# Kernel optimization log

Measured on AMD Instinct MI355X. Metric: run time of the kernel, lower is better.

Reference implementation:

```python
import jax, jax.numpy as jnp
import numpy as np
from functools import partial

B, T, P, W = 32, 4096, 512, 128
NMEL, FILT, PDIM, K = 80, 256, 64, 9
PAD = (K - 1) // 2  # original uses (kernel[0][0]-1)//2 for both convs
EPS = 1e-5


def setup_inputs() -> dict:
    key = jax.random.key(0)
    ks = jax.random.split(key, 8)
    inp = {}
    inp["mask"] = jnp.zeros((B, P), dtype=bool)
    inp["mels"] = jax.random.normal(ks[0], (B, T, NMEL), dtype=jnp.float32)
    inp["mel_mask"] = jnp.zeros((B, T), dtype=bool)
    # uniform segments: 8 frames per phone (sum == T), 4 phones per word (sum == P)
    inp["durations"] = jnp.full((B, P), T // P, dtype=jnp.int32)
    inp["word_phone_len"] = jnp.full((B, W), P // W, dtype=jnp.int32)
    s1 = 1.0 / np.sqrt(NMEL * K)
    s2 = 1.0 / np.sqrt(FILT * K)
    s3 = 1.0 / np.sqrt(FILT)
    inp["conv1_w"] = jax.random.normal(ks[1], (FILT, NMEL, K), dtype=jnp.float32) * s1
    inp["conv1_b"] = jnp.zeros((FILT,), dtype=jnp.float32)
    inp["ln1_g"] = jnp.ones((FILT,), dtype=jnp.float32)
    inp["ln1_b"] = jnp.zeros((FILT,), dtype=jnp.float32)
    inp["conv2_w"] = jax.random.normal(ks[2], (FILT, FILT, K), dtype=jnp.float32) * s2
    inp["conv2_b"] = jnp.zeros((FILT,), dtype=jnp.float32)
    inp["ln2_g"] = jnp.ones((FILT,), dtype=jnp.float32)
    inp["ln2_b"] = jnp.zeros((FILT,), dtype=jnp.float32)
    inp["w1"] = jax.random.normal(ks[3], (FILT, FILT), dtype=jnp.float32) * s3
    inp["b1"] = jnp.zeros((FILT,), dtype=jnp.float32)
    inp["w2"] = jax.random.normal(ks[4], (FILT, PDIM), dtype=jnp.float32) * s3
    inp["b2"] = jnp.zeros((PDIM,), dtype=jnp.float32)
    return inp


def conv1d(x, w, b):
    # x: [B, T, Cin], w: [Cout, Cin, K] -> [B, T, Cout]
    y = jax.lax.conv_general_dilated(x.transpose(0, 2, 1), w, (1,), [(PAD, PAD)])
    return y.transpose(0, 2, 1) + b


def layernorm(x, g, b):
    m = jnp.mean(x, axis=-1, keepdims=True)
    v = jnp.mean(jnp.square(x - m), axis=-1, keepdims=True)
    return (x - m) * jax.lax.rsqrt(v + EPS) * g + b


def seg_mean(feat, lens, n_seg):
    # feat: [L, D], lens: [S] -> [n_seg, D] segment means
    bounds = jnp.cumsum(lens)
    ids = jnp.searchsorted(bounds, jnp.arange(feat.shape[0]), side="right")
    s = jax.ops.segment_sum(feat, ids, num_segments=n_seg)
    cnt = jnp.maximum(lens, 1).astype(feat.dtype)
    return s / cnt[:, None]


def expand_words(word_emb, wlens, n_out):
    # word_emb: [W, D]; scatter each word embedding across its phones -> [n_out, D]
    bounds = jnp.cumsum(wlens)
    wid = jnp.searchsorted(bounds, jnp.arange(n_out), side="right")
    return word_emb[jnp.clip(wid, 0, word_emb.shape[0] - 1)]


def reference(mask, mels, mel_mask, durations, word_phone_len,
              conv1_w, conv1_b, ln1_g, ln1_b, conv2_w, conv2_b, ln2_g, ln2_b,
              w1, b1, w2, b2):
    x = conv1d(mels, conv1_w, conv1_b)
    x = layernorm(jax.nn.relu(x), ln1_g, ln1_b)
    x = conv1d(x, conv2_w, conv2_b)
    x = layernorm(jax.nn.relu(x), ln2_g, ln2_b)  # [B, T, FILT]
    # token-wise (phone) mean pool over mel frames
    x = jax.vmap(partial(seg_mean, n_seg=P))(x, durations)  # [B, P, FILT]
    # word-level mean pool over phones
    x = jax.vmap(partial(seg_mean, n_seg=W))(x, word_phone_len)  # [B, W, FILT]
    x = jax.nn.relu(x @ w1 + b1)
    x = jax.nn.relu(x @ w2 + b2)  # [B, W, PDIM]
    # expand word embeddings back to phone level
    x = jax.vmap(partial(expand_words, n_out=P))(x, word_phone_len)  # [B, P, PDIM]
    x = jnp.where(mask[..., None], 0.0, x)
    return x
```

## Files before the change

### kernel.cpp

```cpp
#include <hip/hip_runtime.h>
#include <hip/hip_fp16.h>
#include <stdint.h>

#define B_ 32
#define T_ 4096
#define P_ 512
#define W_ 128
#define NMEL 80
#define FILT 256
#define PDIM 64
#define KW 9
#define TP8 (T_ + 8)
#define MSTR 104
#define YSTR 264
#define EPS 1e-5f

typedef unsigned short u16;
typedef __attribute__((ext_vector_type(8))) short short8;
typedef __attribute__((ext_vector_type(4))) float f32x4;

typedef const __attribute__((address_space(1))) uint32_t* gptr_t;
typedef __attribute__((address_space(3))) uint32_t* lptr_t;

__device__ __forceinline__ u16 f2h(float v){ return __half_as_ushort(__float2half(v)); }

#define MFMA16(accv, av, bv) \
  asm volatile("v_mfma_f32_16x16x32_f16 %0, %1, %2, %0" : "+v"(accv) : "v"(av), "v"(bv))

__global__ void pack_w(const float* __restrict__ w1, const float* __restrict__ w2,
                       u16* __restrict__ Wp1, u16* __restrict__ Wp2){
  int i = blockIdx.x * 256 + threadIdx.x;
  const int N1 = KW * 12 * FILT;
  const int N2 = KW * 32 * FILT;
  if (i < N1){
    int tap = i / (12*FILT); int r = i - tap*12*FILT; int kg = r / FILT; int co = r - kg*FILT;
    short8 v;
    #pragma unroll
    for (int e=0;e<8;e++){
      int ci = kg*8 + e;
      float x = (ci < NMEL) ? w1[(co*NMEL + ci)*KW + tap] : 0.f;
      v[e] = (short)f2h(x);
    }
    *(short8*)(Wp1 + (size_t)i*8) = v;
  } else if (i < N1 + N2){
    int j = i - N1;
    int tap = j / (32*FILT); int r = j - tap*32*FILT; int kg = r / FILT; int co = r - kg*FILT;
    short8 v;
    #pragma unroll
    for (int e=0;e<8;e++){
      int ci = kg*8 + e;
      v[e] = (short)f2h(w2[(co*FILT + ci)*KW + tap]);
    }
    *(short8*)(Wp2 + (size_t)j*8) = v;
  }
}

__global__ void prep_mels(const float* __restrict__ mels, u16* __restrict__ melsPad){
  int idx = blockIdx.x * 256 + threadIdx.x;
  if (idx >= B_*TP8*MSTR) return;
  int c = idx % MSTR; int r = idx / MSTR; int row = r % TP8; int b = r / TP8;
  float v = 0.f;
  int t = row - 4;
  if (t >= 0 && t < T_ && c < NMEL) v = mels[((size_t)b*T_ + t)*NMEL + c];
  melsPad[idx] = f2h(v);
}

__global__ void prep_seg(const int* __restrict__ dur, const int* __restrict__ wpl,
                         int* __restrict__ dcum, int* __restrict__ wcum,
                         int* __restrict__ pid, int* __restrict__ wid,
                         u16* __restrict__ y1Pad){
  int b = blockIdx.x; int tid = threadIdx.x;
  __shared__ int dc[P_];
  __shared__ int wc[W_];
  if (tid == 0){ int run=0; for (int p=0;p<P_;p++){ run += dur[b*P_+p]; dc[p]=run; dcum[b*P_+p]=run; } }
  if (tid == 1){ int run=0; for (int w=0;w<W_;w++){ run += wpl[b*W_+w]; wc[w]=run; wcum[b*W_+w]=run; } }
  __syncthreads();
  for (int t=tid; t<T_; t+=256){
    int lo=0, hi=P_;
    while (lo < hi){ int mid=(lo+hi)>>1; if (dc[mid] > t) hi=mid; else lo=mid+1; }
    pid[b*T_+t] = lo;
  }
  for (int p=tid; p<P_; p+=256){
    int lo=0, hi=W_;
    while (lo < hi){ int mid=(lo+hi)>>1; if (wc[mid] > p) hi=mid; else lo=mid+1; }
    wid[b*P_+p] = min(lo, W_-1);
  }
  for (int i=tid; i<8*YSTR; i+=256){
    int rr = i / YSTR; int cc = i - rr*YSTR;
    int row = (rr < 4) ? rr : (T_ + rr);
    y1Pad[((size_t)b*TP8 + row)*YSTR + cc] = 0;
  }
}

__global__ __launch_bounds__(256, 2) void conv1_k(
    const u16* __restrict__ melsPad, const u16* __restrict__ Wp1,
    const float* __restrict__ bias, const float* __restrict__ lng,
    const float* __restrict__ lnb, u16* __restrict__ y1Pad){
  __shared__ __align__(16) u16 sA[14336];
  __shared__ __align__(16) u16 sB[2][8192];
  const int tid = threadIdx.x;
  const int wave = tid >> 6, lane = tid & 63, lo = lane & 15, hi = lane >> 4;
  const int b = blockIdx.y, t0 = blockIdx.x * 128;

  {
    const char* gA = (const char*)(melsPad + ((size_t)b*TP8 + t0)*MSTR);
    #pragma unroll
    for (int it=0; it<7; ++it)
      __builtin_amdgcn_global_load_lds((gptr_t)(gA + it*4096 + tid*16),
                                       (lptr_t)((char*)sA + it*4096 + (wave<<10)), 16, 0, 0);
  }
  {
    const char* gW = (const char*)Wp1;
    #pragma unroll
    for (int it=0; it<4; ++it)
      __builtin_amdgcn_global_load_lds((gptr_t)(gW + it*4096 + tid*16),
                                       (lptr_t)((char*)sB[0] + it*4096 + (wave<<10)), 16, 0, 0);
  }

  f32x4 acc[8][4];
  #pragma unroll
  for (int m=0;m<8;m++)
    #pragma unroll
    for (int n=0;n<4;n++) acc[m][n] = (f32x4){0.f,0.f,0.f,0.f};

  __syncthreads();
  for (int cc=0; cc<27; ++cc){
    if (cc < 26){
      int nx = cc + 1;
      const char* gW = (const char*)(Wp1 + (size_t)((nx/3)*12 + (nx%3)*4)*FILT*8);
      char* ldsB = (char*)sB[nx & 1];
      #pragma unroll
      for (int it=0; it<4; ++it)
        __builtin_amdgcn_global_load_lds((gptr_t)(gW + it*4096 + tid*16),
                                         (lptr_t)(ldsB + it*4096 + (wave<<10)), 16, 0, 0);
    }
    const int tap = cc / 3, s = cc % 3;
    const u16* bufB = sB[cc & 1];
    short8 av[8], wv[4];
    #pragma unroll
    for (int m=0;m<8;m++)
      av[m] = *(const short8*)(sA + (m*16 + lo + tap)*MSTR + s*32 + hi*8);
    #pragma unroll
    for (int n=0;n<4;n++)
      wv[n] = *(const short8*)(bufB + ((size_t)hi*FILT + wave*64 + n*16 + lo)*8);
    #pragma unroll
    for (int m=0;m<8;m++)
      #pragma unroll
      for (int n=0;n<4;n++)
        MFMA16(acc[m][n], av[m], wv[n]);
    __syncthreads();
  }
  asm volatile("s_nop 7\n\ts_nop 7" :: );

  float* sred  = (float*)sB;
  float* sred2 = sred + 512;
  float* smean = sred2 + 512;
  float* srstd = smean + 128;

  float bcol[4], gcol[4], btcol[4];
  #pragma unroll
  for (int n=0;n<4;n++){
    int c = wave*64 + n*16 + lo;
    bcol[n]=bias[c]; gcol[n]=lng[c]; btcol[n]=lnb[c];
  }
  #pragma unroll
  for (int m=0;m<8;m++){
    #pragma unroll
    for (int jj=0;jj<4;jj++){
      float s=0.f, q=0.f;
      #pragma unroll
      for (int n=0;n<4;n++){
        float v = fmaxf(acc[m][n][jj] + bcol[n], 0.f);
        s += v; q += v*v;
      }
      #pragma unroll
      for (int off=1; off<16; off<<=1){ s += __shfl_xor(s, off); q += __shfl_xor(q, off); }
      if (lo == 0){ int r = m*16 + hi*4 + jj; sred[r*4+wave] = s; sred2[r*4+wave] = q; }
    }
  }
  __syncthreads();
  if (tid < 128){
    float ss=0.f, qq=0.f;
    #pragma unroll
    for (int w2=0; w2<4; w2++){ ss += sred[tid*4+w2]; qq += sred2[tid*4+w2]; }
    float mean = ss * (1.f/FILT);
    float var  = qq * (1.f/FILT) - mean*mean;
    smean[tid] = mean;
    srstd[tid] = rsqrtf(fmaxf(var, 0.f) + EPS);
  }
  __syncthreads();
  #pragma unroll
  for (int m=0;m<8;m++){
    float mn[4], rs[4];
    #pragma unroll
    for (int jj=0;jj<4;jj++){ int r = m*16+hi*4+jj; mn[jj]=smean[r]; rs[jj]=srstd[r]; }
    #pragma unroll
    for (int jj=0;jj<4;jj++){
      int r = m*16 + hi*4 + jj;
      #pragma unroll
      for (int n=0;n<4;n++){
        float v = fmaxf(acc[m][n][jj] + bcol[n], 0.f);
        float o = (v - mn[jj])*rs[jj]*gcol[n] + btcol[n];
        y1Pad[((size_t)b*TP8 + 4 + t0 + r)*YSTR + wave*64 + n*16 + lo] = f2h(o);
      }
    }
  }
}

__global__ __launch_bounds__(512, 2) void conv2_k(
    const u16* __restrict__ y1Pad, const u16* __restrict__ Wp2,
    const float* __restrict__ bias, const float* __restrict__ lng,
    const float* __restrict__ lnb, const int* __restrict__ pid,
    float* __restrict__ ps){
  __shared__ __align__(16) u16 sA[36864];
  __shared__ __align__(16) u16 sB[2][16384];
  __shared__ int pidT[128];
  const int tid = threadIdx.x;
  const int wave = tid >> 6, lane = tid & 63, lo = lane & 15, hi = lane >> 4;
  const int wr = wave >> 2, wc = wave & 3;
  const int b = blockIdx.y, t0 = blockIdx.x * 128;

  if (tid < 128) pidT[tid] = pid[b*T_ + t0 + tid];
  {
    const char* gA = (const char*)(y1Pad + ((size_t)b*TP8 + t0)*YSTR);
    #pragma unroll
    for (int it=0; it<9; ++it)
      __builtin_amdgcn_global_load_lds((gptr_t)(gA + it*8192 + tid*16),
                                       (lptr_t)((char*)sA + it*8192 + (wave<<10)), 16, 0, 0);
  }
  {
    const char* gW = (const char*)Wp2;
    #pragma unroll
    for (int it=0; it<4; ++it)
      __builtin_amdgcn_global_load_lds((gptr_t)(gW + it*8192 + tid*16),
                                       (lptr_t)((char*)sB[0] + it*8192 + (wave<<10)), 16, 0, 0);
  }

  f32x4 acc[4][4];
  #pragma unroll
  for (int m=0;m<4;m++)
    #pragma unroll
    for (int n=0;n<4;n++) acc[m][n] = (f32x4){0.f,0.f,0.f,0.f};

  __syncthreads();
  for (int cc=0; cc<36; ++cc){
    if (cc < 35){
      int nx = cc + 1;
      const char* gW = (const char*)(Wp2 + (size_t)((nx>>2)*32 + (nx&3)*8)*FILT*8);
      char* ldsB = (char*)sB[nx & 1];
      #pragma unroll
      for (int it=0; it<4; ++it)
        __builtin_amdgcn_global_load_lds((gptr_t)(gW + it*8192 + tid*16),
                                         (lptr_t)(ldsB + it*8192 + (wave<<10)), 16, 0, 0);
    }
    const int tap = cc >> 2, sblk = cc & 3;
    const u16* bufB = sB[cc & 1];
    #pragma unroll
    for (int s2=0; s2<2; ++s2){
      const int sg = sblk*2 + s2;
      short8 av[4], wv[4];
      #pragma unroll
      for (int m=0;m<4;m++)
        av[m] = *(const short8*)(sA + (wr*64 + m*16 + lo + tap)*YSTR + sg*32 + hi*8);
      #pragma unroll
      for (int n=0;n<4;n++)
        wv[n] = *(const short8*)(bufB + ((size_t)(s2*4 + hi)*FILT + wc*64 + n*16 + lo)*8);
      #pragma unroll
      for (int m=0;m<4;m++)
        #pragma unroll
        for (int n=0;n<4;n++)
          MFMA16(acc[m][n], av[m], wv[n]);
    }
    __syncthreads();
  }
  asm volatile("s_nop 7\n\ts_nop 7" :: );

  float* sred  = (float*)sA;
  float* sred2 = sred + 512;
  float* smean = sred2 + 512;
  float* srstd = smean + 128;

  float bcol[4], gcol[4], btcol[4];
  #pragma unroll
  for (int n=0;n<4;n++){
    int c = wc*64 + n*16 + lo;
    bcol[n]=bias[c]; gcol[n]=lng[c]; btcol[n]=lnb[c];
  }
  #pragma unroll
  for (int m=0;m<4;m++){
    #pragma unroll
    for (int jj=0;jj<4;jj++){
      float s=0.f, q=0.f;
      #pragma unroll
      for (int n=0;n<4;n++){
        float v = fmaxf(acc[m][n][jj] + bcol[n], 0.f);
        s += v; q += v*v;
      }
      #pragma unroll
      for (int off=1; off<16; off<<=1){ s += __shfl_xor(s, off); q += __shfl_xor(q, off); }
      if (lo == 0){ int r = wr*64 + m*16 + hi*4 + jj; sred[r*4+wc] = s; sred2[r*4+wc] = q; }
    }
  }
  __syncthreads();
  if (tid < 128){
    float ss=0.f, qq=0.f;
    #pragma unroll
    for (int w2=0; w2<4; w2++){ ss += sred[tid*4+w2]; qq += sred2[tid*4+w2]; }
    float mean = ss * (1.f/FILT);
    float var  = qq * (1.f/FILT) - mean*mean;
    smean[tid] = mean;
    srstd[tid] = rsqrtf(fmaxf(var, 0.f) + EPS);
  }
  __syncthreads();

  #pragma unroll
  for (int m=0;m<4;m++){
    int rbase = wr*64 + m*16 + hi*4;
    int p0v = pidT[rbase], p3v = pidT[rbase+3];
    int fold = (p0v == p3v);
    float mn[4], rs[4];
    #pragma unroll
    for (int jj=0;jj<4;jj++){ int r = rbase+jj; mn[jj]=smean[r]; rs[jj]=srstd[r]; }
    #pragma unroll
    for (int n=0;n<4;n++){
      int c = wc*64 + n*16 + lo;
      float o[4];
      #pragma unroll
      for (int jj=0;jj<4;jj++){
        float v = fmaxf(acc[m][n][jj] + bcol[n], 0.f);
        o[jj] = (v - mn[jj])*rs[jj]*gcol[n] + btcol[n];
      }
      float s4 = fold ? (o[0]+o[1]+o[2]+o[3]) : 0.f;
      float sp = __shfl_xor(s4, 16);
      int   pp = __shfl_xor(p0v, 16);
      int   fp = __shfl_xor(fold, 16);
      float* base = ps + (size_t)b*P_*FILT;
      if (fold){
        if (p0v < P_){
          if (fp && pp == p0v){
            if ((hi & 1) == 0) atomicAdd(base + (size_t)p0v*FILT + c, s4 + sp);
          } else {
            atomicAdd(base + (size_t)p0v*FILT + c, s4);
          }
        }
      } else {
        #pragma unroll
        for (int jj=0;jj<4;jj++){
          int pj = pidT[rbase+jj];
          if (pj < P_) atomicAdd(base + (size_t)pj*FILT + c, o[jj]);
        }
      }
    }
  }
}

#define WPB 8
__global__ __launch_bounds__(256) void word_k(
    const float* __restrict__ ps, const int* __restrict__ dur,
    const int* __restrict__ wcum, const int* __restrict__ wpl,
    const float* __restrict__ w1, const float* __restrict__ b1,
    const float* __restrict__ w2, const float* __restrict__ b2,
    float* __restrict__ wemb){
  int b = blockIdx.y, wg = blockIdx.x * WPB, tid = threadIdx.x;
  __shared__ float wvS[WPB][FILT];
  __shared__ float h1S[WPB][FILT];
  #pragma unroll
  for (int k=0;k<WPB;k++){
    int w = wg + k;
    int p1 = wcum[b*W_ + w]; int p0 = (w == 0) ? 0 : wcum[b*W_ + w - 1];
    if (p1 > P_) p1 = P_;
    int len = wpl[b*W_ + w];
    float a = 0.f;
    for (int p = p0; p < p1; ++p){
      int d = dur[b*P_ + p]; d = d < 1 ? 1 : d;
      a += ps[((size_t)(b*P_ + p))*FILT + tid] / (float)d;
    }
    wvS[k][tid] = a / (float)(len < 1 ? 1 : len);
  }
  __syncthreads();
  float acc[WPB];
  #pragma unroll
  for (int k=0;k<WPB;k++) acc[k] = b1[tid];
  for (int i=0;i<FILT;i++){
    float wcol = w1[i*FILT + tid];
    #pragma unroll
    for (int k=0;k<WPB;k++) acc[k] += wvS[k][i] * wcol;
  }
  #pragma unroll
  for (int k=0;k<WPB;k++) h1S[k][tid] = fmaxf(acc[k], 0.f);
  __syncthreads();
  int c = tid & 63, kq = tid >> 6;
  #pragma unroll
  for (int kk=kq; kk<WPB; kk+=4){
    float u = b2[c];
    for (int i=0;i<FILT;i++) u += h1S[kk][i] * w2[i*PDIM + c];
    wemb[((size_t)(b*W_ + wg + kk))*PDIM + c] = fmaxf(u, 0.f);
  }
}

__global__ void expand_k(const float* __restrict__ wemb, const int* __restrict__ wid,
                         const unsigned char* __restrict__ mask, float* __restrict__ out){
  int idx = blockIdx.x * 256 + threadIdx.x;
  if (idx >= B_*P_*PDIM) return;
  int c = idx & 63; int p = (idx >> 6) & 511; int b = idx >> 15;
  int w = wid[b*P_ + p];
  float v = wemb[((size_t)(b*W_ + w))*PDIM + c];
  if (mask[b*P_ + p]) v = 0.f;
  out[idx] = v;
}

extern "C" void kernel_launch(void* const* d_in, const int* in_sizes, int n_in,
                              void* d_out, int out_size, void* d_ws, size_t ws_size,
                              hipStream_t stream) {
  const unsigned char* mask = (const unsigned char*)d_in[0];
  const float* mels = (const float*)d_in[1];
  const int*   dur  = (const int*)d_in[3];
  const int*   wpl  = (const int*)d_in[4];
  const float* c1w  = (const float*)d_in[5];
  const float* c1b  = (const float*)d_in[6];
  const float* l1g  = (const float*)d_in[7];
  const float* l1b  = (const float*)d_in[8];
  const float* c2w  = (const float*)d_in[9];
  const float* c2b  = (const float*)d_in[10];
  const float* l2g  = (const float*)d_in[11];
  const float* l2b  = (const float*)d_in[12];
  const float* w1   = (const float*)d_in[13];
  const float* b1   = (const float*)d_in[14];
  const float* w2   = (const float*)d_in[15];
  const float* b2   = (const float*)d_in[16];

  char* ws = (char*)d_ws;
  size_t off = 0;
  auto alloc = [&](size_t bytes){ void* p = ws + off; off += (bytes + 255) & ~(size_t)255; return p; };
  u16* melsPad = (u16*)alloc((size_t)B_*TP8*MSTR*2 + 4096);
  u16* y1Pad   = (u16*)alloc((size_t)B_*TP8*YSTR*2 + 4096);
  u16* Wp1     = (u16*)alloc((size_t)KW*12*FILT*8*2);
  u16* Wp2     = (u16*)alloc((size_t)KW*32*FILT*8*2 + 4096);
  int* dcum    = (int*)alloc((size_t)B_*P_*4);
  int* wcum    = (int*)alloc((size_t)B_*W_*4);
  int* pid     = (int*)alloc((size_t)B_*T_*4);
  int* wid     = (int*)alloc((size_t)B_*P_*4);
  float* psum  = (float*)alloc((size_t)B_*P_*FILT*4);
  float* wemb  = (float*)alloc((size_t)B_*W_*PDIM*4);

  hipMemsetAsync(psum, 0, (size_t)B_*P_*FILT*4, stream);
  pack_w<<<(KW*12*FILT + KW*32*FILT + 255)/256, 256, 0, stream>>>(c1w, c2w, Wp1, Wp2);
  prep_mels<<<(B_*TP8*MSTR + 255)/256, 256, 0, stream>>>(mels, melsPad);
  prep_seg<<<B_, 256, 0, stream>>>(dur, wpl, dcum, wcum, pid, wid, y1Pad);
  conv1_k<<<dim3(T_/128, B_), 256, 0, stream>>>(melsPad, Wp1, c1b, l1g, l1b, y1Pad);
  conv2_k<<<dim3(T_/128, B_), 512, 0, stream>>>(y1Pad, Wp2, c2b, l2g, l2b, pid, psum);
  word_k<<<dim3(W_/WPB, B_), 256, 0, stream>>>(psum, dur, wcum, wpl, w1, b1, w2, b2, wemb);
  expand_k<<<(B_*P_*PDIM + 255)/256, 256, 0, stream>>>(wemb, wid, mask, (float*)d_out);
}
```

Before: 355.5 us.

## Per-wave weight staging without block barriers, vectorize prep and expand kernels

The conv1 and conv2 main loops now give each wave its own private LDS ring for weight tiles. Loads are synchronised with explicit vmcnt/lgkmcnt waits instead of a block-wide __syncthreads every K step, and MFMA bursts are issued at raised priority. prep_mels and expand_k are vectorised to 8-half and float4 accesses. prep_seg loads durations in parallel into LDS before the serial scan and drops the unused dcum output. The per-wave staging means each wave fetches its own weight slice, which changes the global traffic pattern, and the hand-placed waitcnt counts must match the number of loads in flight to stay correct.

```diff
diff --git a/kernel.cpp b/kernel.cpp
--- a/kernel.cpp
+++ b/kernel.cpp
@@ -57,23 +57,32 @@
 
 __global__ void prep_mels(const float* __restrict__ mels, u16* __restrict__ melsPad){
   int idx = blockIdx.x * 256 + threadIdx.x;
-  if (idx >= B_*TP8*MSTR) return;
-  int c = idx % MSTR; int r = idx / MSTR; int row = r % TP8; int b = r / TP8;
-  float v = 0.f;
+  if (idx >= B_*TP8*13) return;
+  int ch = idx % 13; int r = idx / 13; int row = r % TP8; int b = r / TP8;
   int t = row - 4;
-  if (t >= 0 && t < T_ && c < NMEL) v = mels[((size_t)b*T_ + t)*NMEL + c];
-  melsPad[idx] = f2h(v);
+  short8 v = (short8){0,0,0,0,0,0,0,0};
+  if (t >= 0 && t < T_ && ch < 10){
+    const float* src = mels + ((size_t)b*T_ + t)*NMEL + ch*8;
+    const f32x4 f0 = *(const f32x4*)src;
+    const f32x4 f1 = *(const f32x4*)(src+4);
+    #pragma unroll
+    for (int j=0;j<4;j++){ v[j]=(short)f2h(f0[j]); v[4+j]=(short)f2h(f1[j]); }
+  }
+  *(short8*)(melsPad + (size_t)idx*8) = v;
 }
 
 __global__ void prep_seg(const int* __restrict__ dur, const int* __restrict__ wpl,
-                         int* __restrict__ dcum, int* __restrict__ wcum,
+                         int* __restrict__ wcum,
                          int* __restrict__ pid, int* __restrict__ wid,
                          u16* __restrict__ y1Pad){
   int b = blockIdx.x; int tid = threadIdx.x;
   __shared__ int dc[P_];
   __shared__ int wc[W_];
-  if (tid == 0){ int run=0; for (int p=0;p<P_;p++){ run += dur[b*P_+p]; dc[p]=run; dcum[b*P_+p]=run; } }
-  if (tid == 1){ int run=0; for (int w=0;w<W_;w++){ run += wpl[b*W_+w]; wc[w]=run; wcum[b*W_+w]=run; } }
+  for (int p=tid; p<P_; p+=256) dc[p] = dur[b*P_+p];
+  if (tid < W_) wc[tid] = wpl[b*W_+tid];
+  __syncthreads();
+  if (tid == 0){ int run=0; for (int p=0;p<P_;p++){ run += dc[p]; dc[p]=run; } }
+  if (tid == 64){ int run=0; for (int w=0;w<W_;w++){ run += wc[w]; wc[w]=run; wcum[b*W_+w]=run; } }
   __syncthreads();
   for (int t=tid; t<T_; t+=256){
     int lo=0, hi=P_;
@@ -97,11 +106,18 @@
     const float* __restrict__ bias, const float* __restrict__ lng,
     const float* __restrict__ lnb, u16* __restrict__ y1Pad){
   __shared__ __align__(16) u16 sA[14336];
-  __shared__ __align__(16) u16 sB[2][8192];
+  __shared__ __align__(16) u16 sR[4][2][2048];
   const int tid = threadIdx.x;
   const int wave = tid >> 6, lane = tid & 63, lo = lane & 15, hi = lane >> 4;
   const int b = blockIdx.y, t0 = blockIdx.x * 128;
 
+  float bcol[4], gcol[4], btcol[4];
+  #pragma unroll
+  for (int n=0;n<4;n++){
+    int c = wave*64 + n*16 + lo;
+    bcol[n]=bias[c]; gcol[n]=lng[c]; btcol[n]=lnb[c];
+  }
+
   {
     const char* gA = (const char*)(melsPad + ((size_t)b*TP8 + t0)*MSTR);
     #pragma unroll
@@ -109,13 +125,21 @@
       __builtin_amdgcn_global_load_lds((gptr_t)(gA + it*4096 + tid*16),
                                        (lptr_t)((char*)sA + it*4096 + (wave<<10)), 16, 0, 0);
   }
-  {
-    const char* gW = (const char*)Wp1;
-    #pragma unroll
-    for (int it=0; it<4; ++it)
-      __builtin_amdgcn_global_load_lds((gptr_t)(gW + it*4096 + tid*16),
-                                       (lptr_t)((char*)sB[0] + it*4096 + (wave<<10)), 16, 0, 0);
-  }
+  const char* gW = (const char*)Wp1 + (size_t)wave*1024;
+  char* myR0 = (char*)&sR[wave][0][0];
+  char* myR1 = (char*)&sR[wave][1][0];
+
+#define C1_STAGE(c, bufp) { \
+    const int tap_ = (c)/3, s_ = (c)%3; \
+    const char* g_ = gW + (size_t)(tap_*12 + s_*4)*4096; \
+    _Pragma("unroll") \
+    for (int j=0;j<4;++j) \
+      __builtin_amdgcn_global_load_lds((gptr_t)(g_ + j*4096 + lane*16), \
+                                       (lptr_t)(bufp + (j<<10)), 16, 0, 0); \
+  }
+
+  C1_STAGE(0, myR0);
+  __syncthreads();
 
   f32x4 acc[8][4];
   #pragma unroll
@@ -123,46 +147,39 @@
     #pragma unroll
     for (int n=0;n<4;n++) acc[m][n] = (f32x4){0.f,0.f,0.f,0.f};
 
-  __syncthreads();
-  for (int cc=0; cc<27; ++cc){
-    if (cc < 26){
-      int nx = cc + 1;
-      const char* gW = (const char*)(Wp1 + (size_t)((nx/3)*12 + (nx%3)*4)*FILT*8);
-      char* ldsB = (char*)sB[nx & 1];
-      #pragma unroll
-      for (int it=0; it<4; ++it)
-        __builtin_amdgcn_global_load_lds((gptr_t)(gW + it*4096 + tid*16),
-                                         (lptr_t)(ldsB + it*4096 + (wave<<10)), 16, 0, 0);
-    }
-    const int tap = cc / 3, s = cc % 3;
-    const u16* bufB = sB[cc & 1];
-    short8 av[8], wv[4];
-    #pragma unroll
-    for (int m=0;m<8;m++)
-      av[m] = *(const short8*)(sA + (m*16 + lo + tap)*MSTR + s*32 + hi*8);
-    #pragma unroll
-    for (int n=0;n<4;n++)
-      wv[n] = *(const short8*)(bufB + ((size_t)hi*FILT + wave*64 + n*16 + lo)*8);
-    #pragma unroll
-    for (int m=0;m<8;m++)
-      #pragma unroll
-      for (int n=0;n<4;n++)
-        MFMA16(acc[m][n], av[m], wv[n]);
-    __syncthreads();
-  }
+#define C1_BODY(cc, WAITI) { \
+    const int tap_ = (cc)/3, s_ = (cc)%3; \
+    char* nbuf = ((cc)&1) ? myR0 : myR1; \
+    if ((cc)+1 < 27) C1_STAGE((cc)+1, nbuf); \
+    asm volatile("s_waitcnt vmcnt(" #WAITI ")" ::: "memory"); \
+    __builtin_amdgcn_sched_barrier(0); \
+    const u16* bufB = (const u16*)(((cc)&1) ? myR1 : myR0); \
+    short8 av[8], wv[4]; \
+    _Pragma("unroll") for (int m=0;m<8;m++) \
+      av[m] = *(const short8*)(sA + (m*16 + lo + tap_)*MSTR + s_*32 + hi*8); \
+    _Pragma("unroll") for (int n=0;n<4;n++) \
+      wv[n] = *(const short8*)(bufB + (hi*64 + n*16 + lo)*8); \
+    asm volatile("s_waitcnt lgkmcnt(0)" ::: "memory"); \
+    __builtin_amdgcn_sched_barrier(0); \
+    __builtin_amdgcn_s_setprio(1); \
+    _Pragma("unroll") for (int m=0;m<8;m++) \
+      _Pragma("unroll") for (int n=0;n<4;n++) \
+        MFMA16(acc[m][n], av[m], wv[n]); \
+    __builtin_amdgcn_s_setprio(0); \
+  }
+
+  #pragma unroll 1
+  for (int cc=0; cc<26; ++cc) C1_BODY(cc, 4)
+  C1_BODY(26, 0)
+
   asm volatile("s_nop 7\n\ts_nop 7" :: );
-
-  float* sred  = (float*)sB;
+  __syncthreads();
+
+  float* sred  = (float*)sR;
   float* sred2 = sred + 512;
   float* smean = sred2 + 512;
   float* srstd = smean + 128;
 
-  float bcol[4], gcol[4], btcol[4];
-  #pragma unroll
-  for (int n=0;n<4;n++){
-    int c = wave*64 + n*16 + lo;
-    bcol[n]=bias[c]; gcol[n]=lng[c]; btcol[n]=lnb[c];
-  }
   #pragma unroll
   for (int m=0;m<8;m++){
     #pragma unroll
@@ -213,14 +230,21 @@
     const float* __restrict__ lnb, const int* __restrict__ pid,
     float* __restrict__ ps){
   __shared__ __align__(16) u16 sA[36864];
-  __shared__ __align__(16) u16 sB[2][16384];
+  __shared__ __align__(16) u16 sR2[8][4][1024];
   __shared__ int pidT[128];
   const int tid = threadIdx.x;
   const int wave = tid >> 6, lane = tid & 63, lo = lane & 15, hi = lane >> 4;
   const int wr = wave >> 2, wc = wave & 3;
   const int b = blockIdx.y, t0 = blockIdx.x * 128;
 
+  float bcol[4], gcol[4], btcol[4];
+  #pragma unroll
+  for (int n=0;n<4;n++){
+    int c = wc*64 + n*16 + lo;
+    bcol[n]=bias[c]; gcol[n]=lng[c]; btcol[n]=lnb[c];
+  }
   if (tid < 128) pidT[tid] = pid[b*T_ + t0 + tid];
+
   {
     const char* gA = (const char*)(y1Pad + ((size_t)b*TP8 + t0)*YSTR);
     #pragma unroll
@@ -228,13 +252,22 @@
       __builtin_amdgcn_global_load_lds((gptr_t)(gA + it*8192 + tid*16),
                                        (lptr_t)((char*)sA + it*8192 + (wave<<10)), 16, 0, 0);
   }
-  {
-    const char* gW = (const char*)Wp2;
-    #pragma unroll
-    for (int it=0; it<4; ++it)
-      __builtin_amdgcn_global_load_lds((gptr_t)(gW + it*8192 + tid*16),
-                                       (lptr_t)((char*)sB[0] + it*8192 + (wave<<10)), 16, 0, 0);
-  }
+  const char* gW2 = (const char*)Wp2 + (size_t)wc*1024;
+  char* myR = (char*)&sR2[wave][0][0];
+  const int laneOff2 = ((lane>>5)<<12) | ((lane&31)<<4);
+
+#define C2_STAGE(c) { \
+    const int ks2 = (c)>>1, nh2 = (c)&1; \
+    const int tap2 = ks2>>3, sg2 = ks2&7; \
+    const char* g_ = gW2 + (size_t)((tap2*32 + sg2*4)*256)*16 + nh2*512; \
+    char* d_ = myR + (((c)&3)<<11); \
+    __builtin_amdgcn_global_load_lds((gptr_t)(g_ + laneOff2), (lptr_t)(d_), 16, 0, 0); \
+    __builtin_amdgcn_global_load_lds((gptr_t)(g_ + 8192 + laneOff2), (lptr_t)(d_ + 1024), 16, 0, 0); \
+  }
+
+  C2_STAGE(0)
+  C2_STAGE(1)
+  __syncthreads();
 
   f32x4 acc[4][4];
   #pragma unroll
@@ -242,50 +275,50 @@
     #pragma unroll
     for (int n=0;n<4;n++) acc[m][n] = (f32x4){0.f,0.f,0.f,0.f};
 
-  __syncthreads();
-  for (int cc=0; cc<36; ++cc){
-    if (cc < 35){
-      int nx = cc + 1;
-      const char* gW = (const char*)(Wp2 + (size_t)((nx>>2)*32 + (nx&3)*8)*FILT*8);
-      char* ldsB = (char*)sB[nx & 1];
-      #pragma unroll
-      for (int it=0; it<4; ++it)
-        __builtin_amdgcn_global_load_lds((gptr_t)(gW + it*8192 + tid*16),
-                                         (lptr_t)(ldsB + it*8192 + (wave<<10)), 16, 0, 0);
-    }
-    const int tap = cc >> 2, sblk = cc & 3;
-    const u16* bufB = sB[cc & 1];
-    #pragma unroll
-    for (int s2=0; s2<2; ++s2){
-      const int sg = sblk*2 + s2;
-      short8 av[4], wv[4];
-      #pragma unroll
-      for (int m=0;m<4;m++)
-        av[m] = *(const short8*)(sA + (wr*64 + m*16 + lo + tap)*YSTR + sg*32 + hi*8);
-      #pragma unroll
-      for (int n=0;n<4;n++)
-        wv[n] = *(const short8*)(bufB + ((size_t)(s2*4 + hi)*FILT + wc*64 + n*16 + lo)*8);
-      #pragma unroll
-      for (int m=0;m<4;m++)
-        #pragma unroll
-        for (int n=0;n<4;n++)
-          MFMA16(acc[m][n], av[m], wv[n]);
-    }
-    __syncthreads();
-  }
+#define C2_KS(ks, W0, W1) { \
+    const int tap_ = (ks)>>3, sg_ = (ks)&7; \
+    const int c0 = 2*(ks); \
+    if (c0+2 < 144) C2_STAGE(c0+2) \
+    asm volatile("s_waitcnt vmcnt(" #W0 ")" ::: "memory"); \
+    __builtin_amdgcn_sched_barrier(0); \
+    short8 av[4], wv0[2], wv1[2]; \
+    const u16* bA = sA + (wr*64 + lo + tap_)*YSTR + sg_*32 + hi*8; \
+    _Pragma("unroll") for (int m=0;m<4;m++) av[m] = *(const short8*)(bA + m*16*YSTR); \
+    const u16* bB0 = (const u16*)(myR + ((c0&3)<<11)); \
+    _Pragma("unroll") for (int n=0;n<2;n++) wv0[n] = *(const short8*)(bB0 + (hi*32 + n*16 + lo)*8); \
+    asm volatile("s_waitcnt lgkmcnt(0)" ::: "memory"); \
+    __builtin_amdgcn_sched_barrier(0); \
+    __builtin_amdgcn_s_setprio(1); \
+    _Pragma("unroll") for (int m=0;m<4;m++) \
+      _Pragma("unroll") for (int n=0;n<2;n++) \
+        MFMA16(acc[m][n], av[m], wv0[n]); \
+    __builtin_amdgcn_s_setprio(0); \
+    if (c0+3 < 144) C2_STAGE(c0+3) \
+    asm volatile("s_waitcnt vmcnt(" #W1 ")" ::: "memory"); \
+    __builtin_amdgcn_sched_barrier(0); \
+    const u16* bB1 = (const u16*)(myR + (((c0+1)&3)<<11)); \
+    _Pragma("unroll") for (int n=0;n<2;n++) wv1[n] = *(const short8*)(bB1 + (hi*32 + n*16 + lo)*8); \
+    asm volatile("s_waitcnt lgkmcnt(0)" ::: "memory"); \
+    __builtin_amdgcn_sched_barrier(0); \
+    __builtin_amdgcn_s_setprio(1); \
+    _Pragma("unroll") for (int m=0;m<4;m++) \
+      _Pragma("unroll") for (int n=0;n<2;n++) \
+        MFMA16(acc[m][n+2], av[m], wv1[n]); \
+    __builtin_amdgcn_s_setprio(0); \
+  }
+
+  #pragma unroll 1
+  for (int ks=0; ks<71; ++ks) C2_KS(ks, 4, 4)
+  C2_KS(71, 2, 0)
+
   asm volatile("s_nop 7\n\ts_nop 7" :: );
+  __syncthreads();
 
   float* sred  = (float*)sA;
   float* sred2 = sred + 512;
   float* smean = sred2 + 512;
   float* srstd = smean + 128;
 
-  float bcol[4], gcol[4], btcol[4];
-  #pragma unroll
-  for (int n=0;n<4;n++){
-    int c = wc*64 + n*16 + lo;
-    bcol[n]=bias[c]; gcol[n]=lng[c]; btcol[n]=lnb[c];
-  }
   #pragma unroll
   for (int m=0;m<4;m++){
     #pragma unroll
@@ -401,12 +434,12 @@
 __global__ void expand_k(const float* __restrict__ wemb, const int* __restrict__ wid,
                          const unsigned char* __restrict__ mask, float* __restrict__ out){
   int idx = blockIdx.x * 256 + threadIdx.x;
-  if (idx >= B_*P_*PDIM) return;
-  int c = idx & 63; int p = (idx >> 6) & 511; int b = idx >> 15;
-  int w = wid[b*P_ + p];
-  float v = wemb[((size_t)(b*W_ + w))*PDIM + c];
-  if (mask[b*P_ + p]) v = 0.f;
-  out[idx] = v;
+  if (idx >= B_*P_*16) return;
+  int q = idx & 15; int p = (idx >> 4) & 511; int bb = idx >> 13;
+  int w = wid[bb*P_ + p];
+  f32x4 v = *(const f32x4*)(wemb + ((size_t)(bb*W_ + w))*PDIM + q*4);
+  if (mask[bb*P_ + p]) v = (f32x4){0.f,0.f,0.f,0.f};
+  *(f32x4*)(out + (size_t)idx*4) = v;
 }
 
 extern "C" void kernel_launch(void* const* d_in, const int* in_sizes, int n_in,
@@ -436,7 +469,6 @@
   u16* y1Pad   = (u16*)alloc((size_t)B_*TP8*YSTR*2 + 4096);
   u16* Wp1     = (u16*)alloc((size_t)KW*12*FILT*8*2);
   u16* Wp2     = (u16*)alloc((size_t)KW*32*FILT*8*2 + 4096);
-  int* dcum    = (int*)alloc((size_t)B_*P_*4);
   int* wcum    = (int*)alloc((size_t)B_*W_*4);
   int* pid     = (int*)alloc((size_t)B_*T_*4);
   int* wid     = (int*)alloc((size_t)B_*P_*4);
@@ -445,10 +477,10 @@
 
   hipMemsetAsync(psum, 0, (size_t)B_*P_*FILT*4, stream);
   pack_w<<<(KW*12*FILT + KW*32*FILT + 255)/256, 256, 0, stream>>>(c1w, c2w, Wp1, Wp2);
-  prep_mels<<<(B_*TP8*MSTR + 255)/256, 256, 0, stream>>>(mels, melsPad);
-  prep_seg<<<B_, 256, 0, stream>>>(dur, wpl, dcum, wcum, pid, wid, y1Pad);
+  prep_mels<<<(B_*TP8*13 + 255)/256, 256, 0, stream>>>(mels, melsPad);
+  prep_seg<<<B_, 256, 0, stream>>>(dur, wpl, wcum, pid, wid, y1Pad);
   conv1_k<<<dim3(T_/128, B_), 256, 0, stream>>>(melsPad, Wp1, c1b, l1g, l1b, y1Pad);
   conv2_k<<<dim3(T_/128, B_), 512, 0, stream>>>(y1Pad, Wp2, c2b, l2g, l2b, pid, psum);
   word_k<<<dim3(W_/WPB, B_), 256, 0, stream>>>(psum, dur, wcum, wpl, w1, b1, w2, b2, wemb);
-  expand_k<<<(B_*P_*PDIM + 255)/256, 256, 0, stream>>>(wemb, wid, mask, (float*)d_out);
-}
+  expand_k<<<(B_*P_*16 + 255)/256, 256, 0, stream>>>(wemb, wid, mask, (float*)d_out);
+}
```

Result: slower. 416.8 us (+17.2%).
